# Performance work log

Hardware: AMD Instinct MI355X
Metric: run time of the kernel (lower is better)

The kernel has to match this reference:

```python
import jax, jax.numpy as jnp
import numpy as np

N_NODES = 50000
N_EDGES = 800000
IN_DIM, HIDDEN, Z_DIM = 32, 64, 32


def gcn_conv(x, W, b, src, dst, n):
    """PyG-style GCNConv: h = D^{-1/2}(A+I)D^{-1/2} (x W) + b."""
    h = x @ W  # [N, out]
    loop = jnp.arange(n, dtype=src.dtype)
    s = jnp.concatenate([src, loop])  # add self-loops
    d = jnp.concatenate([dst, loop])
    deg = jax.ops.segment_sum(jnp.ones(s.shape, h.dtype), d, num_segments=n)
    dinv = jax.lax.rsqrt(jnp.maximum(deg, jnp.asarray(1.0, h.dtype)))
    norm = dinv[s] * dinv[d]                       # [E+N]
    msg = h[s] * norm[:, None]                     # gather + scale
    out = jax.ops.segment_sum(msg, d, num_segments=n)  # scatter-add
    return out + b


def setup_inputs() -> dict:
    key = jax.random.key(0)
    ks = jax.random.split(key, 8)
    sc = lambda fan_in: 1.0 / np.sqrt(fan_in)
    x = jax.random.normal(ks[0], (N_NODES, IN_DIM), jnp.float32)
    edge_index = jax.random.randint(ks[1], (2, N_EDGES), 0, N_NODES, jnp.int64)
    W1 = jax.random.normal(ks[2], (IN_DIM, HIDDEN), jnp.float32) * sc(IN_DIM)
    b1 = jnp.zeros((HIDDEN,), jnp.float32)
    W2 = jax.random.normal(ks[3], (HIDDEN, HIDDEN), jnp.float32) * sc(HIDDEN)
    b2 = jnp.zeros((HIDDEN,), jnp.float32)
    W_mu = jax.random.normal(ks[4], (HIDDEN, Z_DIM), jnp.float32) * sc(HIDDEN)
    b_mu = jnp.zeros((Z_DIM,), jnp.float32)
    W_lv = jax.random.normal(ks[5], (HIDDEN, Z_DIM), jnp.float32) * sc(HIDDEN)
    b_lv = jnp.zeros((Z_DIM,), jnp.float32)
    eps = jax.random.normal(ks[6], (N_NODES, Z_DIM), jnp.float32)
    return {"x": x, "edge_index": edge_index, "W1": W1, "b1": b1, "W2": W2,
            "b2": b2, "W_mu": W_mu, "b_mu": b_mu, "W_lv": W_lv, "b_lv": b_lv,
            "eps": eps}


def reference(x, edge_index, W1, b1, W2, b2, W_mu, b_mu, W_lv, b_lv, eps):
    src, dst = edge_index[0], edge_index[1]
    n = x.shape[0]
    h = jax.nn.relu(gcn_conv(x, W1, b1, src, dst, n))
    h = jax.nn.relu(gcn_conv(h, W2, b2, src, dst, n))
    # dropout p=0.0 -> identity
    mu = gcn_conv(h, W_mu, b_mu, src, dst, n)
    logvar = gcn_conv(h, W_lv, b_lv, src, dst, n)
    z = mu + jnp.exp(0.5 * logvar) * eps  # reparametrize
    return (z, mu, logvar)
```

## Files before the change

kernel.cpp:

```cpp
#include <hip/hip_runtime.h>
#include <math.h>

#define N_NODES 50000
#define N_EDGES 800000
#define IN_DIM 32
#define HIDDEN 64
#define Z_DIM 32
#define SCAN_B 256
#define NB_SCAN ((N_NODES + SCAN_B - 1) / SCAN_B)
#define N_XCD 8
#define NPX ((N_NODES + N_XCD - 1) / N_XCD)
#define SLICE 2048
#define N_SLICE ((N_EDGES + SLICE - 1) / SLICE)
#define SCAT_B (N_SLICE * N_XCD)
#define FB 2048
#define CPAD 16

__device__ __forceinline__ float bf2f(unsigned short u) {
    return __uint_as_float(((unsigned int)u) << 16);
}
__device__ __forceinline__ unsigned short f2bf(float f) {
    unsigned int u = __float_as_uint(f);
    u += 0x7fffu + ((u >> 16) & 1u);
    return (unsigned short)(u >> 16);
}

__device__ __forceinline__ int detect64(const int* raw) {
    int lane = threadIdx.x & 63;
    int odd = raw[2 * lane + 1];
    unsigned long long b = __ballot(odd != 0);
    return (b == 0ULL) ? 1 : 0;
}

__global__ void prep_a_kernel(const float* __restrict__ x, unsigned short* __restrict__ xb,
                              const void* __restrict__ raw, int2* __restrict__ ep0,
                              int* __restrict__ dstc) {
    int is64 = detect64((const int*)raw);
    int i = blockIdx.x * 256 + threadIdx.x;
    if (i < N_NODES * IN_DIM) xb[i] = f2bf(x[i]);
    if (i < N_EDGES) {
        int s, d;
        if (is64) {
            s = (int)((const long long*)raw)[i];
            d = (int)((const long long*)raw)[N_EDGES + i];
        } else {
            s = ((const int*)raw)[i];
            d = ((const int*)raw)[N_EDGES + i];
        }
        ep0[i] = make_int2(s, d);
        dstc[i] = d;
    }
}

__global__ __launch_bounds__(256) void hist_kernel(const int* __restrict__ dstc,
                                                   int* __restrict__ cnt,
                                                   unsigned short* __restrict__ rank) {
    int xcd = blockIdx.x % N_XCD;
    int sl  = blockIdx.x / N_XCD;
    int lo  = xcd * NPX, hi = lo + NPX;
    int base = sl * SLICE;
#pragma unroll
    for (int j = 0; j < SLICE / 256; j++) {
        int e = base + j * 256 + threadIdx.x;
        if (e < N_EDGES) {
            int d = dstc[e];
            if (d >= lo && d < hi)
                rank[e] = (unsigned short)atomicAdd(&cnt[(size_t)d * CPAD], 1);
        }
    }
}

__global__ void scan1_kernel(const int* __restrict__ cnt, int* __restrict__ pre,
                             int* __restrict__ bsum, float* __restrict__ dinv) {
    __shared__ int s[SCAN_B];
    int t = threadIdx.x;
    int g = blockIdx.x * SCAN_B + t;
    int v = (g < N_NODES) ? cnt[(size_t)g * CPAD] : 0;
    if (g < N_NODES) dinv[g] = rsqrtf((float)(v + 1));
    s[t] = v;
    __syncthreads();
    for (int o = 1; o < SCAN_B; o <<= 1) {
        int add = (t >= o) ? s[t - o] : 0;
        __syncthreads();
        s[t] += add;
        __syncthreads();
    }
    if (g < N_NODES) pre[g] = s[t] - v;
    if (t == SCAN_B - 1) bsum[blockIdx.x] = s[t];
}

__global__ void scan23_kernel(int* __restrict__ rowptr, const int* __restrict__ bsum) {
    __shared__ int s[256];
    int t = threadIdx.x;
    int v = (t < NB_SCAN) ? bsum[t] : 0;
    s[t] = v;
    __syncthreads();
    for (int o = 1; o < 256; o <<= 1) {
        int add = (t >= o) ? s[t - o] : 0;
        __syncthreads();
        s[t] += add;
        __syncthreads();
    }
    int excl = s[blockIdx.x] - bsum[blockIdx.x];
    int g = blockIdx.x * SCAN_B + t;
    if (g < N_NODES) rowptr[g] += excl;
    if (g == 0) rowptr[N_NODES] = N_EDGES;
}

__global__ __launch_bounds__(256) void scatter_kernel(
        const int2* __restrict__ ep0, const unsigned short* __restrict__ rank,
        const int* __restrict__ rowptr, const float* __restrict__ dinv,
        int2* __restrict__ ep) {
    int base = blockIdx.x * SLICE;
#pragma unroll
    for (int j = 0; j < SLICE / 256; j++) {
        int e = base + j * 256 + threadIdx.x;
        if (e < N_EDGES) {
            int2 sd = ep0[e];
            int p = rowptr[sd.y] + (int)rank[e];
            ep[p] = make_int2(sd.x, __float_as_int(dinv[sd.x]));
        }
    }
}

__device__ __forceinline__ void agg_body64(int e0, int e1, int2 pr,
                                           const int2* __restrict__ ep,
                                           const uint2* __restrict__ g2,
                                           int lane, float acc[4]) {
    int gsel = lane >> 4;
    int c    = lane & 15;
    for (int base = e0; base < e1; base += 64) {
        int cnt = e1 - base; cnt = cnt > 64 ? 64 : cnt;
        for (int j = 0; j < cnt; j += 16) {
            uint2 fv[4]; float wv[4];
#pragma unroll
            for (int u = 0; u < 4; u++) {
                int idx = j + u * 4 + gsel;
                int cl  = idx < cnt ? idx : cnt - 1;
                int s   = __builtin_amdgcn_ds_bpermute(cl << 2, pr.x);
                int w   = __builtin_amdgcn_ds_bpermute(cl << 2, pr.y);
                wv[u]   = idx < cnt ? __int_as_float(w) : 0.0f;
                fv[u]   = g2[(size_t)s * 16 + c];
            }
#pragma unroll
            for (int u = 0; u < 4; u++) {
                acc[0] = fmaf(wv[u], __uint_as_float(fv[u].x << 16),         acc[0]);
                acc[1] = fmaf(wv[u], __uint_as_float(fv[u].x & 0xffff0000u), acc[1]);
                acc[2] = fmaf(wv[u], __uint_as_float(fv[u].y << 16),         acc[2]);
                acc[3] = fmaf(wv[u], __uint_as_float(fv[u].y & 0xffff0000u), acc[3]);
            }
        }
        int nb = base + 64;
        if (nb + lane < e1) pr = ep[nb + lane];
    }
}

__device__ __forceinline__ void agg_body32(int e0, int e1, int2 pr,
                                           const int2* __restrict__ ep,
                                           const uint2* __restrict__ x2,
                                           int lane, float acc[4]) {
    int gsel = lane >> 3;
    int c    = lane & 7;
    for (int base = e0; base < e1; base += 64) {
        int cnt = e1 - base; cnt = cnt > 64 ? 64 : cnt;
        for (int j = 0; j < cnt; j += 16) {
            uint2 fv[2]; float wv[2];
#pragma unroll
            for (int u = 0; u < 2; u++) {
                int idx = j + u * 8 + gsel;
                int cl  = idx < cnt ? idx : cnt - 1;
                int s   = __builtin_amdgcn_ds_bpermute(cl << 2, pr.x);
                int w   = __builtin_amdgcn_ds_bpermute(cl << 2, pr.y);
                wv[u]   = idx < cnt ? __int_as_float(w) : 0.0f;
                fv[u]   = x2[(size_t)s * 8 + c];
            }
#pragma unroll
            for (int u = 0; u < 2; u++) {
                acc[0] = fmaf(wv[u], __uint_as_float(fv[u].x << 16),         acc[0]);
                acc[1] = fmaf(wv[u], __uint_as_float(fv[u].x & 0xffff0000u), acc[1]);
                acc[2] = fmaf(wv[u], __uint_as_float(fv[u].y << 16),         acc[2]);
                acc[3] = fmaf(wv[u], __uint_as_float(fv[u].y & 0xffff0000u), acc[3]);
            }
        }
        int nb = base + 64;
        if (nb + lane < e1) pr = ep[nb + lane];
    }
}

__global__ __launch_bounds__(256, 4) void fused_layer32_kernel(
        const int* __restrict__ rowptr, const int2* __restrict__ ep,
        const float* __restrict__ dinv, const unsigned short* __restrict__ xb,
        const float* __restrict__ W1, const float* __restrict__ b1,
        unsigned short* __restrict__ out) {
    __shared__ float sq[4 * 32];
    int lane = threadIdx.x & 63;
    int wav  = threadIdx.x >> 6;
    int gsel = lane >> 3;
    int c    = lane & 7;
    const uint2* x2 = (const uint2*)xb;
    float wcol[IN_DIM];
#pragma unroll
    for (int k = 0; k < IN_DIM; k++) wcol[k] = W1[k * 64 + lane];
    float bb = b1[lane];
    int wid = __builtin_amdgcn_readfirstlane((int)((blockIdx.x * blockDim.x + threadIdx.x) >> 6));
    int nw  = (gridDim.x * blockDim.x) >> 6;
    int v = wid;
    if (v >= N_NODES) return;
    int e0 = rowptr[v], e1 = rowptr[v + 1];
    float dv = dinv[v];
    uint2 hv = x2[(size_t)v * 8 + c];
    int2 pr = make_int2(0, 0);
    if (lane < e1 - e0) pr = ep[e0 + lane];
    while (v < N_NODES) {
        int vn = v + nw;
        int e0n = 0, e1n = 0;
        float dvn = 0.0f;
        uint2 hvn = make_uint2(0, 0);
        int2 prn = make_int2(0, 0);
        if (vn < N_NODES) {
            e0n = rowptr[vn]; e1n = rowptr[vn + 1];
            dvn = dinv[vn];
            hvn = x2[(size_t)vn * 8 + c];
            if (lane < e1n - e0n) prn = ep[e0n + lane];
        }
        float sv = (gsel == 0) ? dv : 0.0f;
        float acc[4];
        acc[0] = sv * __uint_as_float(hv.x << 16);
        acc[1] = sv * __uint_as_float(hv.x & 0xffff0000u);
        acc[2] = sv * __uint_as_float(hv.y << 16);
        acc[3] = sv * __uint_as_float(hv.y & 0xffff0000u);
        agg_body32(e0, e1, pr, ep, x2, lane, acc);
#pragma unroll
        for (int i = 0; i < 4; i++) {
            acc[i] += __shfl_xor(acc[i], 8);
            acc[i] += __shfl_xor(acc[i], 16);
            acc[i] += __shfl_xor(acc[i], 32);
        }
        if (lane < 8)
            ((float4*)(sq + wav * 32))[c] =
                make_float4(dv * acc[0], dv * acc[1], dv * acc[2], dv * acc[3]);
        float o = bb;
        const float4* q4 = (const float4*)(sq + wav * 32);
#pragma unroll
        for (int k = 0; k < IN_DIM / 4; k++) {
            float4 t = q4[k];
            o = fmaf(t.x, wcol[4 * k + 0], o);
            o = fmaf(t.y, wcol[4 * k + 1], o);
            o = fmaf(t.z, wcol[4 * k + 2], o);
            o = fmaf(t.w, wcol[4 * k + 3], o);
        }
        out[(size_t)v * 64 + lane] = f2bf(fmaxf(o, 0.0f));
        v = vn; e0 = e0n; e1 = e1n; dv = dvn; hv = hvn; pr = prn;
    }
}

__global__ __launch_bounds__(256, 4) void fused_layer64_kernel(
        const int* __restrict__ rowptr, const int2* __restrict__ ep,
        const float* __restrict__ dinv, const unsigned short* __restrict__ g,
        const float* __restrict__ W, const float* __restrict__ bias,
        unsigned short* __restrict__ out) {
    __shared__ float sq[4 * 64];
    int lane = threadIdx.x & 63;
    int wav  = threadIdx.x >> 6;
    int gsel = lane >> 4;
    int c    = lane & 15;
    const uint2* g2 = (const uint2*)g;
    float wcol[HIDDEN];
#pragma unroll
    for (int k = 0; k < HIDDEN; k++) wcol[k] = W[k * 64 + lane];
    float bb = bias[lane];
    int wid = __builtin_amdgcn_readfirstlane((int)((blockIdx.x * blockDim.x + threadIdx.x) >> 6));
    int nw  = (gridDim.x * blockDim.x) >> 6;
    int v = wid;
    if (v >= N_NODES) return;
    int e0 = rowptr[v], e1 = rowptr[v + 1];
    float dv = dinv[v];
    uint2 hv = g2[(size_t)v * 16 + c];
    int2 pr = make_int2(0, 0);
    if (lane < e1 - e0) pr = ep[e0 + lane];
    while (v < N_NODES) {
        int vn = v + nw;
        int e0n = 0, e1n = 0;
        float dvn = 0.0f;
        uint2 hvn = make_uint2(0, 0);
        int2 prn = make_int2(0, 0);
        if (vn < N_NODES) {
            e0n = rowptr[vn]; e1n = rowptr[vn + 1];
            dvn = dinv[vn];
            hvn = g2[(size_t)vn * 16 + c];
            if (lane < e1n - e0n) prn = ep[e0n + lane];
        }
        float sv = (gsel == 0) ? dv : 0.0f;
        float acc[4];
        acc[0] = sv * __uint_as_float(hv.x << 16);
        acc[1] = sv * __uint_as_float(hv.x & 0xffff0000u);
        acc[2] = sv * __uint_as_float(hv.y << 16);
        acc[3] = sv * __uint_as_float(hv.y & 0xffff0000u);
        agg_body64(e0, e1, pr, ep, g2, lane, acc);
#pragma unroll
        for (int i = 0; i < 4; i++) {
            acc[i] += __shfl_xor(acc[i], 16);
            acc[i] += __shfl_xor(acc[i], 32);
        }
        if (lane < 16)
            ((float4*)(sq + wav * 64))[c] =
                make_float4(dv * acc[0], dv * acc[1], dv * acc[2], dv * acc[3]);
        float o = bb;
        const float4* q4 = (const float4*)(sq + wav * 64);
#pragma unroll
        for (int k = 0; k < HIDDEN / 4; k++) {
            float4 t = q4[k];
            o = fmaf(t.x, wcol[4 * k + 0], o);
            o = fmaf(t.y, wcol[4 * k + 1], o);
            o = fmaf(t.z, wcol[4 * k + 2], o);
            o = fmaf(t.w, wcol[4 * k + 3], o);
        }
        out[(size_t)v * 64 + lane] = f2bf(fmaxf(o, 0.0f));
        v = vn; e0 = e0n; e1 = e1n; dv = dvn; hv = hvn; pr = prn;
    }
}

__global__ __launch_bounds__(256, 4) void fused_head_kernel(
        const int* __restrict__ rowptr, const int2* __restrict__ ep,
        const float* __restrict__ dinv, const unsigned short* __restrict__ g,
        const float* __restrict__ Wmu, const float* __restrict__ Wlv,
        const float* __restrict__ bmu, const float* __restrict__ blv,
        const float* __restrict__ eps, float* __restrict__ outz) {
    __shared__ float sq[4 * 64];
    int lane = threadIdx.x & 63;
    int wav  = threadIdx.x >> 6;
    int gsel = lane >> 4;
    int c    = lane & 15;
    int f = lane & 31;
    bool hi = lane >= 32;
    const uint2* g2 = (const uint2*)g;
    float wcol[HIDDEN];
#pragma unroll
    for (int k = 0; k < HIDDEN; k++)
        wcol[k] = hi ? Wlv[k * 32 + f] : Wmu[k * 32 + f];
    float bb = hi ? blv[f] : bmu[f];
    float* z  = outz;
    float* mu = outz + (size_t)N_NODES * Z_DIM;
    float* lv = outz + 2 * (size_t)N_NODES * Z_DIM;
    int wid = __builtin_amdgcn_readfirstlane((int)((blockIdx.x * blockDim.x + threadIdx.x) >> 6));
    int nw  = (gridDim.x * blockDim.x) >> 6;
    int v = wid;
    if (v >= N_NODES) return;
    int e0 = rowptr[v], e1 = rowptr[v + 1];
    float dv = dinv[v];
    uint2 hv = g2[(size_t)v * 16 + c];
    int2 pr = make_int2(0, 0);
    if (lane < e1 - e0) pr = ep[e0 + lane];
    while (v < N_NODES) {
        int vn = v + nw;
        int e0n = 0, e1n = 0;
        float dvn = 0.0f;
        uint2 hvn = make_uint2(0, 0);
        int2 prn = make_int2(0, 0);
        if (vn < N_NODES) {
            e0n = rowptr[vn]; e1n = rowptr[vn + 1];
            dvn = dinv[vn];
            hvn = g2[(size_t)vn * 16 + c];
            if (lane < e1n - e0n) prn = ep[e0n + lane];
        }
        float sv = (gsel == 0) ? dv : 0.0f;
        float acc[4];
        acc[0] = sv * __uint_as_float(hv.x << 16);
        acc[1] = sv * __uint_as_float(hv.x & 0xffff0000u);
        acc[2] = sv * __uint_as_float(hv.y << 16);
        acc[3] = sv * __uint_as_float(hv.y & 0xffff0000u);
        agg_body64(e0, e1, pr, ep, g2, lane, acc);
#pragma unroll
        for (int i = 0; i < 4; i++) {
            acc[i] += __shfl_xor(acc[i], 16);
            acc[i] += __shfl_xor(acc[i], 32);
        }
        if (lane < 16)
            ((float4*)(sq + wav * 64))[c] =
                make_float4(dv * acc[0], dv * acc[1], dv * acc[2], dv * acc[3]);
        float m = bb;
        const float4* q4 = (const float4*)(sq + wav * 64);
#pragma unroll
        for (int k = 0; k < HIDDEN / 4; k++) {
            float4 t = q4[k];
            m = fmaf(t.x, wcol[4 * k + 0], m);
            m = fmaf(t.y, wcol[4 * k + 1], m);
            m = fmaf(t.z, wcol[4 * k + 2], m);
            m = fmaf(t.w, wcol[4 * k + 3], m);
        }
        float ev = eps[(size_t)v * Z_DIM + f];
        float t  = expf(0.5f * m) * ev;
        float tlo = __shfl(t, lane | 32);
        size_t o = (size_t)v * Z_DIM + f;
        if (!hi) { mu[o] = m; z[o] = m + tlo; }
        else     { lv[o] = m; }
        v = vn; e0 = e0n; e1 = e1n; dv = dvn; hv = hvn; pr = prn;
    }
}

extern "C" void kernel_launch(void* const* d_in, const int* in_sizes, int n_in,
                              void* d_out, int out_size, void* d_ws, size_t ws_size,
                              hipStream_t stream) {
    const float* x   = (const float*)d_in[0];
    const void*  ei  = d_in[1];
    const float* W1  = (const float*)d_in[2];
    const float* b1  = (const float*)d_in[3];
    const float* W2  = (const float*)d_in[4];
    const float* b2  = (const float*)d_in[5];
    const float* Wmu = (const float*)d_in[6];
    const float* bmu = (const float*)d_in[7];
    const float* Wlv = (const float*)d_in[8];
    const float* blv = (const float*)d_in[9];
    const float* eps = (const float*)d_in[10];
    float* out = (float*)d_out;
    (void)in_sizes; (void)n_in; (void)out_size; (void)ws_size;

    char* ws = (char*)d_ws;
    size_t off = 0;
    auto alloc = [&](size_t bytes) -> void* {
        void* p = ws + off;
        off += (bytes + 255) & ~(size_t)255;
        return p;
    };
    int2*           ep     = (int2*)alloc(sizeof(int2) * N_EDGES);
    int2*           ep0    = (int2*)alloc(sizeof(int2) * N_EDGES);
    int*            dstc   = (int*)alloc(sizeof(int) * N_EDGES);
    unsigned short* rank   = (unsigned short*)alloc(sizeof(short) * N_EDGES);
    int*            rowptr = (int*)alloc(sizeof(int) * (N_NODES + 1));
    int*            cnt    = (int*)alloc(sizeof(int) * (size_t)N_NODES * CPAD);
    float*          dinv   = (float*)alloc(sizeof(float) * N_NODES);
    int*            bsum   = (int*)alloc(sizeof(int) * 256);
    unsigned short* xb     = (unsigned short*)alloc(sizeof(short) * (size_t)N_NODES * IN_DIM);
    unsigned short* G      = (unsigned short*)alloc(sizeof(short) * (size_t)N_NODES * HIDDEN);
    unsigned short* H      = (unsigned short*)alloc(sizeof(short) * (size_t)N_NODES * HIDDEN);

    hipMemsetAsync(cnt, 0, sizeof(int) * (size_t)N_NODES * CPAD, stream);
    prep_a_kernel<<<(N_NODES * IN_DIM + 255) / 256, 256, 0, stream>>>(x, xb, ei, ep0, dstc);
    hist_kernel<<<SCAT_B, 256, 0, stream>>>(dstc, cnt, rank);
    scan1_kernel<<<NB_SCAN, SCAN_B, 0, stream>>>(cnt, rowptr, bsum, dinv);
    scan23_kernel<<<NB_SCAN, SCAN_B, 0, stream>>>(rowptr, bsum);
    scatter_kernel<<<N_SLICE, 256, 0, stream>>>(ep0, rank, rowptr, dinv, ep);
    fused_layer32_kernel<<<FB, 256, 0, stream>>>(rowptr, ep, dinv, xb, W1, b1, H);
    fused_layer64_kernel<<<FB, 256, 0, stream>>>(rowptr, ep, dinv, H, W2, b2, G);
    fused_head_kernel<<<FB, 256, 0, stream>>>(rowptr, ep, dinv, G, Wmu, Wlv, bmu, blv, eps, out);
}
```

Measured before the change: 234.1 us.

## Process two nodes per wave in aggregation and compact edge staging

The three fused GCN layer kernels now aggregate two destination nodes per wavefront in an interleaved loop, and they prefetch the next pair's state. This doubles the number of independent gathers in flight, to hide memory latency, and drops the occupancy hint from launch bounds. Edge staging packs src/dst as ushort2, which relies on node ids staying below 65536. The separate dst copy is removed, and zeroing the counters is folded into the prep kernel instead of a memset. The costs are higher register pressure and wasted lanes when the two nodes' degrees differ.

```diff
diff --git a/kernel.cpp b/kernel.cpp
--- a/kernel.cpp
+++ b/kernel.cpp
@@ -16,9 +16,6 @@
 #define FB 2048
 #define CPAD 16
 
-__device__ __forceinline__ float bf2f(unsigned short u) {
-    return __uint_as_float(((unsigned int)u) << 16);
-}
 __device__ __forceinline__ unsigned short f2bf(float f) {
     unsigned int u = __float_as_uint(f);
     u += 0x7fffu + ((u >> 16) & 1u);
@@ -33,11 +30,12 @@
 }
 
 __global__ void prep_a_kernel(const float* __restrict__ x, unsigned short* __restrict__ xb,
-                              const void* __restrict__ raw, int2* __restrict__ ep0,
-                              int* __restrict__ dstc) {
+                              const void* __restrict__ raw, ushort2* __restrict__ ep0,
+                              int* __restrict__ cnt) {
     int is64 = detect64((const int*)raw);
     int i = blockIdx.x * 256 + threadIdx.x;
     if (i < N_NODES * IN_DIM) xb[i] = f2bf(x[i]);
+    if (i < N_NODES * CPAD) cnt[i] = 0;
     if (i < N_EDGES) {
         int s, d;
         if (is64) {
@@ -47,12 +45,11 @@
             s = ((const int*)raw)[i];
             d = ((const int*)raw)[N_EDGES + i];
         }
-        ep0[i] = make_int2(s, d);
-        dstc[i] = d;
-    }
-}
-
-__global__ __launch_bounds__(256) void hist_kernel(const int* __restrict__ dstc,
+        ep0[i] = make_ushort2((unsigned short)s, (unsigned short)d);
+    }
+}
+
+__global__ __launch_bounds__(256) void hist_kernel(const ushort2* __restrict__ ep0,
                                                    int* __restrict__ cnt,
                                                    unsigned short* __restrict__ rank) {
     int xcd = blockIdx.x % N_XCD;
@@ -63,14 +60,14 @@
     for (int j = 0; j < SLICE / 256; j++) {
         int e = base + j * 256 + threadIdx.x;
         if (e < N_EDGES) {
-            int d = dstc[e];
+            int d = ep0[e].y;
             if (d >= lo && d < hi)
                 rank[e] = (unsigned short)atomicAdd(&cnt[(size_t)d * CPAD], 1);
         }
     }
 }
 
-__global__ void scan1_kernel(const int* __restrict__ cnt, int* __restrict__ pre,
+__global__ void scan1_kernel(const int* __restrict__ cnt, int* __restrict__ rowptr,
                              int* __restrict__ bsum, float* __restrict__ dinv) {
     __shared__ int s[SCAN_B];
     int t = threadIdx.x;
@@ -85,7 +82,7 @@
         s[t] += add;
         __syncthreads();
     }
-    if (g < N_NODES) pre[g] = s[t] - v;
+    if (g < N_NODES) rowptr[g] = s[t] - v;
     if (t == SCAN_B - 1) bsum[blockIdx.x] = s[t];
 }
 
@@ -108,7 +105,7 @@
 }
 
 __global__ __launch_bounds__(256) void scatter_kernel(
-        const int2* __restrict__ ep0, const unsigned short* __restrict__ rank,
+        const ushort2* __restrict__ ep0, const unsigned short* __restrict__ rank,
         const int* __restrict__ rowptr, const float* __restrict__ dinv,
         int2* __restrict__ ep) {
     int base = blockIdx.x * SLICE;
@@ -116,83 +113,114 @@
     for (int j = 0; j < SLICE / 256; j++) {
         int e = base + j * 256 + threadIdx.x;
         if (e < N_EDGES) {
-            int2 sd = ep0[e];
+            ushort2 sd = ep0[e];
             int p = rowptr[sd.y] + (int)rank[e];
-            ep[p] = make_int2(sd.x, __float_as_int(dinv[sd.x]));
-        }
-    }
-}
-
-__device__ __forceinline__ void agg_body64(int e0, int e1, int2 pr,
-                                           const int2* __restrict__ ep,
-                                           const uint2* __restrict__ g2,
-                                           int lane, float acc[4]) {
-    int gsel = lane >> 4;
-    int c    = lane & 15;
-    for (int base = e0; base < e1; base += 64) {
-        int cnt = e1 - base; cnt = cnt > 64 ? 64 : cnt;
-        for (int j = 0; j < cnt; j += 16) {
-            uint2 fv[4]; float wv[4];
+            int s = sd.x;
+            ep[p] = make_int2(s, __float_as_int(dinv[s]));
+        }
+    }
+}
+
+__device__ __forceinline__ void agg_dual64(
+        int e0A, int e1A, int2 prA, int e0B, int e1B, int2 prB,
+        const int2* __restrict__ ep, const uint2* __restrict__ g2,
+        int lane, int gsel, int c, float accA[4], float accB[4]) {
+    int bA = e0A, bB = e0B;
+    while (bA < e1A || bB < e1B) {
+        int cA = e1A - bA; cA = cA < 0 ? 0 : (cA > 64 ? 64 : cA);
+        int cB = e1B - bB; cB = cB < 0 ? 0 : (cB > 64 ? 64 : cB);
+        int mj = cA > cB ? cA : cB;
+        for (int j = 0; j < mj; j += 16) {
+            uint2 fA[4], fB[4]; float wA[4], wB[4];
 #pragma unroll
             for (int u = 0; u < 4; u++) {
                 int idx = j + u * 4 + gsel;
-                int cl  = idx < cnt ? idx : cnt - 1;
-                int s   = __builtin_amdgcn_ds_bpermute(cl << 2, pr.x);
-                int w   = __builtin_amdgcn_ds_bpermute(cl << 2, pr.y);
-                wv[u]   = idx < cnt ? __int_as_float(w) : 0.0f;
-                fv[u]   = g2[(size_t)s * 16 + c];
+                int clA = idx < cA ? idx : (cA > 0 ? cA - 1 : 0);
+                int clB = idx < cB ? idx : (cB > 0 ? cB - 1 : 0);
+                int sA  = __builtin_amdgcn_ds_bpermute(clA << 2, prA.x);
+                int wwA = __builtin_amdgcn_ds_bpermute(clA << 2, prA.y);
+                int sB  = __builtin_amdgcn_ds_bpermute(clB << 2, prB.x);
+                int wwB = __builtin_amdgcn_ds_bpermute(clB << 2, prB.y);
+                wA[u] = idx < cA ? __int_as_float(wwA) : 0.0f;
+                wB[u] = idx < cB ? __int_as_float(wwB) : 0.0f;
+                fA[u] = g2[(size_t)sA * 16 + c];
+                fB[u] = g2[(size_t)sB * 16 + c];
             }
 #pragma unroll
             for (int u = 0; u < 4; u++) {
-                acc[0] = fmaf(wv[u], __uint_as_float(fv[u].x << 16),         acc[0]);
-                acc[1] = fmaf(wv[u], __uint_as_float(fv[u].x & 0xffff0000u), acc[1]);
-                acc[2] = fmaf(wv[u], __uint_as_float(fv[u].y << 16),         acc[2]);
-                acc[3] = fmaf(wv[u], __uint_as_float(fv[u].y & 0xffff0000u), acc[3]);
+                accA[0] = fmaf(wA[u], __uint_as_float(fA[u].x << 16),         accA[0]);
+                accA[1] = fmaf(wA[u], __uint_as_float(fA[u].x & 0xffff0000u), accA[1]);
+                accA[2] = fmaf(wA[u], __uint_as_float(fA[u].y << 16),         accA[2]);
+                accA[3] = fmaf(wA[u], __uint_as_float(fA[u].y & 0xffff0000u), accA[3]);
+                accB[0] = fmaf(wB[u], __uint_as_float(fB[u].x << 16),         accB[0]);
+                accB[1] = fmaf(wB[u], __uint_as_float(fB[u].x & 0xffff0000u), accB[1]);
+                accB[2] = fmaf(wB[u], __uint_as_float(fB[u].y << 16),         accB[2]);
+                accB[3] = fmaf(wB[u], __uint_as_float(fB[u].y & 0xffff0000u), accB[3]);
             }
         }
-        int nb = base + 64;
-        if (nb + lane < e1) pr = ep[nb + lane];
-    }
-}
-
-__device__ __forceinline__ void agg_body32(int e0, int e1, int2 pr,
-                                           const int2* __restrict__ ep,
-                                           const uint2* __restrict__ x2,
-                                           int lane, float acc[4]) {
-    int gsel = lane >> 3;
-    int c    = lane & 7;
-    for (int base = e0; base < e1; base += 64) {
-        int cnt = e1 - base; cnt = cnt > 64 ? 64 : cnt;
-        for (int j = 0; j < cnt; j += 16) {
-            uint2 fv[2]; float wv[2];
+        bA += 64; bB += 64;
+        if (bA < e1A) { int i2 = bA + lane; prA = ep[i2 < e1A ? i2 : e1A - 1]; }
+        if (bB < e1B) { int i2 = bB + lane; prB = ep[i2 < e1B ? i2 : e1B - 1]; }
+    }
+}
+
+__device__ __forceinline__ void agg_dual32(
+        int e0A, int e1A, int2 prA, int e0B, int e1B, int2 prB,
+        const int2* __restrict__ ep, const uint2* __restrict__ x2,
+        int lane, int gsel, int c, float accA[4], float accB[4]) {
+    int bA = e0A, bB = e0B;
+    while (bA < e1A || bB < e1B) {
+        int cA = e1A - bA; cA = cA < 0 ? 0 : (cA > 64 ? 64 : cA);
+        int cB = e1B - bB; cB = cB < 0 ? 0 : (cB > 64 ? 64 : cB);
+        int mj = cA > cB ? cA : cB;
+        for (int j = 0; j < mj; j += 16) {
+            uint2 fA[2], fB[2]; float wA[2], wB[2];
 #pragma unroll
             for (int u = 0; u < 2; u++) {
                 int idx = j + u * 8 + gsel;
-                int cl  = idx < cnt ? idx : cnt - 1;
-                int s   = __builtin_amdgcn_ds_bpermute(cl << 2, pr.x);
-                int w   = __builtin_amdgcn_ds_bpermute(cl << 2, pr.y);
-                wv[u]   = idx < cnt ? __int_as_float(w) : 0.0f;
-                fv[u]   = x2[(size_t)s * 8 + c];
+                int clA = idx < cA ? idx : (cA > 0 ? cA - 1 : 0);
+                int clB = idx < cB ? idx : (cB > 0 ? cB - 1 : 0);
+                int sA  = __builtin_amdgcn_ds_bpermute(clA << 2, prA.x);
+                int wwA = __builtin_amdgcn_ds_bpermute(clA << 2, prA.y);
+                int sB  = __builtin_amdgcn_ds_bpermute(clB << 2, prB.x);
+                int wwB = __builtin_amdgcn_ds_bpermute(clB << 2, prB.y);
+                wA[u] = idx < cA ? __int_as_float(wwA) : 0.0f;
+                wB[u] = idx < cB ? __int_as_float(wwB) : 0.0f;
+                fA[u] = x2[(size_t)sA * 8 + c];
+                fB[u] = x2[(size_t)sB * 8 + c];
             }
 #pragma unroll
             for (int u = 0; u < 2; u++) {
-                acc[0] = fmaf(wv[u], __uint_as_float(fv[u].x << 16),         acc[0]);
-                acc[1] = fmaf(wv[u], __uint_as_float(fv[u].x & 0xffff0000u), acc[1]);
-                acc[2] = fmaf(wv[u], __uint_as_float(fv[u].y << 16),         acc[2]);
-                acc[3] = fmaf(wv[u], __uint_as_float(fv[u].y & 0xffff0000u), acc[3]);
+                accA[0] = fmaf(wA[u], __uint_as_float(fA[u].x << 16),         accA[0]);
+                accA[1] = fmaf(wA[u], __uint_as_float(fA[u].x & 0xffff0000u), accA[1]);
+                accA[2] = fmaf(wA[u], __uint_as_float(fA[u].y << 16),         accA[2]);
+                accA[3] = fmaf(wA[u], __uint_as_float(fA[u].y & 0xffff0000u), accA[3]);
+                accB[0] = fmaf(wB[u], __uint_as_float(fB[u].x << 16),         accB[0]);
+                accB[1] = fmaf(wB[u], __uint_as_float(fB[u].x & 0xffff0000u), accB[1]);
+                accB[2] = fmaf(wB[u], __uint_as_float(fB[u].y << 16),         accB[2]);
+                accB[3] = fmaf(wB[u], __uint_as_float(fB[u].y & 0xffff0000u), accB[3]);
             }
         }
-        int nb = base + 64;
-        if (nb + lane < e1) pr = ep[nb + lane];
-    }
-}
-
-__global__ __launch_bounds__(256, 4) void fused_layer32_kernel(
+        bA += 64; bB += 64;
+        if (bA < e1A) { int i2 = bA + lane; prA = ep[i2 < e1A ? i2 : e1A - 1]; }
+        if (bB < e1B) { int i2 = bB + lane; prB = ep[i2 < e1B ? i2 : e1B - 1]; }
+    }
+}
+
+#define LOAD_STATE(v, e0, e1, dv, hv, pr, HLOAD)                            \
+    {                                                                       \
+        e0 = rowptr[v]; e1 = rowptr[v + 1];                                 \
+        dv = dinv[v];                                                       \
+        hv = HLOAD;                                                         \
+        if (lane < e1 - e0) pr = ep[e0 + lane];                             \
+    }
+
+__global__ __launch_bounds__(256) void fused_layer32_kernel(
         const int* __restrict__ rowptr, const int2* __restrict__ ep,
         const float* __restrict__ dinv, const unsigned short* __restrict__ xb,
         const float* __restrict__ W1, const float* __restrict__ b1,
         unsigned short* __restrict__ out) {
-    __shared__ float sq[4 * 32];
+    __shared__ float sq[4][2][IN_DIM];
     int lane = threadIdx.x & 63;
     int wav  = threadIdx.x >> 6;
     int gsel = lane >> 3;
@@ -204,62 +232,87 @@
     float bb = b1[lane];
     int wid = __builtin_amdgcn_readfirstlane((int)((blockIdx.x * blockDim.x + threadIdx.x) >> 6));
     int nw  = (gridDim.x * blockDim.x) >> 6;
-    int v = wid;
-    if (v >= N_NODES) return;
-    int e0 = rowptr[v], e1 = rowptr[v + 1];
-    float dv = dinv[v];
-    uint2 hv = x2[(size_t)v * 8 + c];
-    int2 pr = make_int2(0, 0);
-    if (lane < e1 - e0) pr = ep[e0 + lane];
-    while (v < N_NODES) {
-        int vn = v + nw;
-        int e0n = 0, e1n = 0;
-        float dvn = 0.0f;
-        uint2 hvn = make_uint2(0, 0);
-        int2 prn = make_int2(0, 0);
-        if (vn < N_NODES) {
-            e0n = rowptr[vn]; e1n = rowptr[vn + 1];
-            dvn = dinv[vn];
-            hvn = x2[(size_t)vn * 8 + c];
-            if (lane < e1n - e0n) prn = ep[e0n + lane];
-        }
-        float sv = (gsel == 0) ? dv : 0.0f;
-        float acc[4];
-        acc[0] = sv * __uint_as_float(hv.x << 16);
-        acc[1] = sv * __uint_as_float(hv.x & 0xffff0000u);
-        acc[2] = sv * __uint_as_float(hv.y << 16);
-        acc[3] = sv * __uint_as_float(hv.y & 0xffff0000u);
-        agg_body32(e0, e1, pr, ep, x2, lane, acc);
+    int vA = wid;
+    if (vA >= N_NODES) return;
+    int e0A = 0, e1A = 0, e0B = 0, e1B = 0;
+    float dvA = 0.0f, dvB = 0.0f;
+    uint2 hvA = make_uint2(0, 0), hvB = make_uint2(0, 0);
+    int2 prA = make_int2(0, 0), prB = make_int2(0, 0);
+    LOAD_STATE(vA, e0A, e1A, dvA, hvA, prA, x2[(size_t)vA * 8 + c])
+    {
+        int vB = vA + nw;
+        if (vB < N_NODES)
+            LOAD_STATE(vB, e0B, e1B, dvB, hvB, prB, x2[(size_t)vB * 8 + c])
+    }
+    while (vA < N_NODES) {
+        int vB = vA + nw;
+        int vA2 = vA + 2 * nw;
+        int e0A2 = 0, e1A2 = 0, e0B2 = 0, e1B2 = 0;
+        float dvA2 = 0.0f, dvB2 = 0.0f;
+        uint2 hvA2 = make_uint2(0, 0), hvB2 = make_uint2(0, 0);
+        int2 prA2 = make_int2(0, 0), prB2 = make_int2(0, 0);
+        if (vA2 < N_NODES)
+            LOAD_STATE(vA2, e0A2, e1A2, dvA2, hvA2, prA2, x2[(size_t)vA2 * 8 + c])
+        if (vA2 + nw < N_NODES) {
+            int vB2 = vA2 + nw;
+            LOAD_STATE(vB2, e0B2, e1B2, dvB2, hvB2, prB2, x2[(size_t)vB2 * 8 + c])
+        }
+        float svA = (gsel == 0) ? dvA : 0.0f;
+        float svB = (gsel == 0) ? dvB : 0.0f;
+        float accA[4], accB[4];
+        accA[0] = svA * __uint_as_float(hvA.x << 16);
+        accA[1] = svA * __uint_as_float(hvA.x & 0xffff0000u);
+        accA[2] = svA * __uint_as_float(hvA.y << 16);
+        accA[3] = svA * __uint_as_float(hvA.y & 0xffff0000u);
+        accB[0] = svB * __uint_as_float(hvB.x << 16);
+        accB[1] = svB * __uint_as_float(hvB.x & 0xffff0000u);
+        accB[2] = svB * __uint_as_float(hvB.y << 16);
+        accB[3] = svB * __uint_as_float(hvB.y & 0xffff0000u);
+        agg_dual32(e0A, e1A, prA, e0B, e1B, prB, ep, x2, lane, gsel, c, accA, accB);
 #pragma unroll
         for (int i = 0; i < 4; i++) {
-            acc[i] += __shfl_xor(acc[i], 8);
-            acc[i] += __shfl_xor(acc[i], 16);
-            acc[i] += __shfl_xor(acc[i], 32);
-        }
-        if (lane < 8)
-            ((float4*)(sq + wav * 32))[c] =
-                make_float4(dv * acc[0], dv * acc[1], dv * acc[2], dv * acc[3]);
-        float o = bb;
-        const float4* q4 = (const float4*)(sq + wav * 32);
+            accA[i] += __shfl_xor(accA[i], 8);
+            accA[i] += __shfl_xor(accA[i], 16);
+            accA[i] += __shfl_xor(accA[i], 32);
+            accB[i] += __shfl_xor(accB[i], 8);
+            accB[i] += __shfl_xor(accB[i], 16);
+            accB[i] += __shfl_xor(accB[i], 32);
+        }
+        if (lane < 8) {
+            ((float4*)(&sq[wav][0][0]))[c] =
+                make_float4(dvA * accA[0], dvA * accA[1], dvA * accA[2], dvA * accA[3]);
+            ((float4*)(&sq[wav][1][0]))[c] =
+                make_float4(dvB * accB[0], dvB * accB[1], dvB * accB[2], dvB * accB[3]);
+        }
+        float oA = bb, oB = bb;
+        const float4* qA = (const float4*)(&sq[wav][0][0]);
+        const float4* qB = (const float4*)(&sq[wav][1][0]);
 #pragma unroll
         for (int k = 0; k < IN_DIM / 4; k++) {
-            float4 t = q4[k];
-            o = fmaf(t.x, wcol[4 * k + 0], o);
-            o = fmaf(t.y, wcol[4 * k + 1], o);
-            o = fmaf(t.z, wcol[4 * k + 2], o);
-            o = fmaf(t.w, wcol[4 * k + 3], o);
-        }
-        out[(size_t)v * 64 + lane] = f2bf(fmaxf(o, 0.0f));
-        v = vn; e0 = e0n; e1 = e1n; dv = dvn; hv = hvn; pr = prn;
-    }
-}
-
-__global__ __launch_bounds__(256, 4) void fused_layer64_kernel(
+            float4 ta = qA[k], tb = qB[k];
+            oA = fmaf(ta.x, wcol[4 * k + 0], oA);
+            oA = fmaf(ta.y, wcol[4 * k + 1], oA);
+            oA = fmaf(ta.z, wcol[4 * k + 2], oA);
+            oA = fmaf(ta.w, wcol[4 * k + 3], oA);
+            oB = fmaf(tb.x, wcol[4 * k + 0], oB);
+            oB = fmaf(tb.y, wcol[4 * k + 1], oB);
+            oB = fmaf(tb.z, wcol[4 * k + 2], oB);
+            oB = fmaf(tb.w, wcol[4 * k + 3], oB);
+        }
+        out[(size_t)vA * 64 + lane] = f2bf(fmaxf(oA, 0.0f));
+        if (vB < N_NODES) out[(size_t)vB * 64 + lane] = f2bf(fmaxf(oB, 0.0f));
+        vA = vA2;
+        e0A = e0A2; e1A = e1A2; dvA = dvA2; hvA = hvA2; prA = prA2;
+        e0B = e0B2; e1B = e1B2; dvB = dvB2; hvB = hvB2; prB = prB2;
+    }
+}
+
+__global__ __launch_bounds__(256) void fused_layer64_kernel(
         const int* __restrict__ rowptr, const int2* __restrict__ ep,
         const float* __restrict__ dinv, const unsigned short* __restrict__ g,
         const float* __restrict__ W, const float* __restrict__ bias,
         unsigned short* __restrict__ out) {
-    __shared__ float sq[4 * 64];
+    __shared__ float sq[4][2][HIDDEN];
     int lane = threadIdx.x & 63;
     int wav  = threadIdx.x >> 6;
     int gsel = lane >> 4;
@@ -271,62 +324,86 @@
     float bb = bias[lane];
     int wid = __builtin_amdgcn_readfirstlane((int)((blockIdx.x * blockDim.x + threadIdx.x) >> 6));
     int nw  = (gridDim.x * blockDim.x) >> 6;
-    int v = wid;
-    if (v >= N_NODES) return;
-    int e0 = rowptr[v], e1 = rowptr[v + 1];
-    float dv = dinv[v];
-    uint2 hv = g2[(size_t)v * 16 + c];
-    int2 pr = make_int2(0, 0);
-    if (lane < e1 - e0) pr = ep[e0 + lane];
-    while (v < N_NODES) {
-        int vn = v + nw;
-        int e0n = 0, e1n = 0;
-        float dvn = 0.0f;
-        uint2 hvn = make_uint2(0, 0);
-        int2 prn = make_int2(0, 0);
-        if (vn < N_NODES) {
-            e0n = rowptr[vn]; e1n = rowptr[vn + 1];
-            dvn = dinv[vn];
-            hvn = g2[(size_t)vn * 16 + c];
-            if (lane < e1n - e0n) prn = ep[e0n + lane];
-        }
-        float sv = (gsel == 0) ? dv : 0.0f;
-        float acc[4];
-        acc[0] = sv * __uint_as_float(hv.x << 16);
-        acc[1] = sv * __uint_as_float(hv.x & 0xffff0000u);
-        acc[2] = sv * __uint_as_float(hv.y << 16);
-        acc[3] = sv * __uint_as_float(hv.y & 0xffff0000u);
-        agg_body64(e0, e1, pr, ep, g2, lane, acc);
+    int vA = wid;
+    if (vA >= N_NODES) return;
+    int e0A = 0, e1A = 0, e0B = 0, e1B = 0;
+    float dvA = 0.0f, dvB = 0.0f;
+    uint2 hvA = make_uint2(0, 0), hvB = make_uint2(0, 0);
+    int2 prA = make_int2(0, 0), prB = make_int2(0, 0);
+    LOAD_STATE(vA, e0A, e1A, dvA, hvA, prA, g2[(size_t)vA * 16 + c])
+    {
+        int vB = vA + nw;
+        if (vB < N_NODES)
+            LOAD_STATE(vB, e0B, e1B, dvB, hvB, prB, g2[(size_t)vB * 16 + c])
+    }
+    while (vA < N_NODES) {
+        int vB = vA + nw;
+        int vA2 = vA + 2 * nw;
+        int e0A2 = 0, e1A2 = 0, e0B2 = 0, e1B2 = 0;
+        float dvA2 = 0.0f, dvB2 = 0.0f;
+        uint2 hvA2 = make_uint2(0, 0), hvB2 = make_uint2(0, 0);
+        int2 prA2 = make_int2(0, 0), prB2 = make_int2(0, 0);
+        if (vA2 < N_NODES)
+            LOAD_STATE(vA2, e0A2, e1A2, dvA2, hvA2, prA2, g2[(size_t)vA2 * 16 + c])
+        if (vA2 + nw < N_NODES) {
+            int vB2 = vA2 + nw;
+            LOAD_STATE(vB2, e0B2, e1B2, dvB2, hvB2, prB2, g2[(size_t)vB2 * 16 + c])
+        }
+        float svA = (gsel == 0) ? dvA : 0.0f;
+        float svB = (gsel == 0) ? dvB : 0.0f;
+        float accA[4], accB[4];
+        accA[0] = svA * __uint_as_float(hvA.x << 16);
+        accA[1] = svA * __uint_as_float(hvA.x & 0xffff0000u);
+        accA[2] = svA * __uint_as_float(hvA.y << 16);
+        accA[3] = svA * __uint_as_float(hvA.y & 0xffff0000u);
+        accB[0] = svB * __uint_as_float(hvB.x << 16);
+        accB[1] = svB * __uint_as_float(hvB.x & 0xffff0000u);
+        accB[2] = svB * __uint_as_float(hvB.y << 16);
+        accB[3] = svB * __uint_as_float(hvB.y & 0xffff0000u);
+        agg_dual64(e0A, e1A, prA, e0B, e1B, prB, ep, g2, lane, gsel, c, accA, accB);
 #pragma unroll
         for (int i = 0; i < 4; i++) {
-            acc[i] += __shfl_xor(acc[i], 16);
-            acc[i] += __shfl_xor(acc[i], 32);
-        }
-        if (lane < 16)
-            ((float4*)(sq + wav * 64))[c] =
-                make_float4(dv * acc[0], dv * acc[1], dv * acc[2], dv * acc[3]);
-        float o = bb;
-        const float4* q4 = (const float4*)(sq + wav * 64);
+            accA[i] += __shfl_xor(accA[i], 16);
+            accA[i] += __shfl_xor(accA[i], 32);
+            accB[i] += __shfl_xor(accB[i], 16);
+            accB[i] += __shfl_xor(accB[i], 32);
+        }
+        if (lane < 16) {
+            ((float4*)(&sq[wav][0][0]))[c] =
+                make_float4(dvA * accA[0], dvA * accA[1], dvA * accA[2], dvA * accA[3]);
+            ((float4*)(&sq[wav][1][0]))[c] =
+                make_float4(dvB * accB[0], dvB * accB[1], dvB * accB[2], dvB * accB[3]);
+        }
+        float oA = bb, oB = bb;
+        const float4* qA = (const float4*)(&sq[wav][0][0]);
+        const float4* qB = (const float4*)(&sq[wav][1][0]);
 #pragma unroll
         for (int k = 0; k < HIDDEN / 4; k++) {
-            float4 t = q4[k];
-            o = fmaf(t.x, wcol[4 * k + 0], o);
-            o = fmaf(t.y, wcol[4 * k + 1], o);
-            o = fmaf(t.z, wcol[4 * k + 2], o);
-            o = fmaf(t.w, wcol[4 * k + 3], o);
-        }
-        out[(size_t)v * 64 + lane] = f2bf(fmaxf(o, 0.0f));
-        v = vn; e0 = e0n; e1 = e1n; dv = dvn; hv = hvn; pr = prn;
-    }
-}
-
-__global__ __launch_bounds__(256, 4) void fused_head_kernel(
+            float4 ta = qA[k], tb = qB[k];
+            oA = fmaf(ta.x, wcol[4 * k + 0], oA);
+            oA = fmaf(ta.y, wcol[4 * k + 1], oA);
+            oA = fmaf(ta.z, wcol[4 * k + 2], oA);
+            oA = fmaf(ta.w, wcol[4 * k + 3], oA);
+            oB = fmaf(tb.x, wcol[4 * k + 0], oB);
+            oB = fmaf(tb.y, wcol[4 * k + 1], oB);
+            oB = fmaf(tb.z, wcol[4 * k + 2], oB);
+            oB = fmaf(tb.w, wcol[4 * k + 3], oB);
+        }
+        out[(size_t)vA * 64 + lane] = f2bf(fmaxf(oA, 0.0f));
+        if (vB < N_NODES) out[(size_t)vB * 64 + lane] = f2bf(fmaxf(oB, 0.0f));
+        vA = vA2;
+        e0A = e0A2; e1A = e1A2; dvA = dvA2; hvA = hvA2; prA = prA2;
+        e0B = e0B2; e1B = e1B2; dvB = dvB2; hvB = hvB2; prB = prB2;
+    }
+}
+
+__global__ __launch_bounds__(256) void fused_head_kernel(
         const int* __restrict__ rowptr, const int2* __restrict__ ep,
         const float* __restrict__ dinv, const unsigned short* __restrict__ g,
         const float* __restrict__ Wmu, const float* __restrict__ Wlv,
         const float* __restrict__ bmu, const float* __restrict__ blv,
         const float* __restrict__ eps, float* __restrict__ outz) {
-    __shared__ float sq[4 * 64];
+    __shared__ float sq[4][2][HIDDEN];
     int lane = threadIdx.x & 63;
     int wav  = threadIdx.x >> 6;
     int gsel = lane >> 4;
@@ -344,57 +421,90 @@
     float* lv = outz + 2 * (size_t)N_NODES * Z_DIM;
     int wid = __builtin_amdgcn_readfirstlane((int)((blockIdx.x * blockDim.x + threadIdx.x) >> 6));
     int nw  = (gridDim.x * blockDim.x) >> 6;
-    int v = wid;
-    if (v >= N_NODES) return;
-    int e0 = rowptr[v], e1 = rowptr[v + 1];
-    float dv = dinv[v];
-    uint2 hv = g2[(size_t)v * 16 + c];
-    int2 pr = make_int2(0, 0);
-    if (lane < e1 - e0) pr = ep[e0 + lane];
-    while (v < N_NODES) {
-        int vn = v + nw;
-        int e0n = 0, e1n = 0;
-        float dvn = 0.0f;
-        uint2 hvn = make_uint2(0, 0);
-        int2 prn = make_int2(0, 0);
-        if (vn < N_NODES) {
-            e0n = rowptr[vn]; e1n = rowptr[vn + 1];
-            dvn = dinv[vn];
-            hvn = g2[(size_t)vn * 16 + c];
-            if (lane < e1n - e0n) prn = ep[e0n + lane];
-        }
-        float sv = (gsel == 0) ? dv : 0.0f;
-        float acc[4];
-        acc[0] = sv * __uint_as_float(hv.x << 16);
-        acc[1] = sv * __uint_as_float(hv.x & 0xffff0000u);
-        acc[2] = sv * __uint_as_float(hv.y << 16);
-        acc[3] = sv * __uint_as_float(hv.y & 0xffff0000u);
-        agg_body64(e0, e1, pr, ep, g2, lane, acc);
+    int vA = wid;
+    if (vA >= N_NODES) return;
+    int e0A = 0, e1A = 0, e0B = 0, e1B = 0;
+    float dvA = 0.0f, dvB = 0.0f;
+    uint2 hvA = make_uint2(0, 0), hvB = make_uint2(0, 0);
+    int2 prA = make_int2(0, 0), prB = make_int2(0, 0);
+    LOAD_STATE(vA, e0A, e1A, dvA, hvA, prA, g2[(size_t)vA * 16 + c])
+    {
+        int vB = vA + nw;
+        if (vB < N_NODES)
+            LOAD_STATE(vB, e0B, e1B, dvB, hvB, prB, g2[(size_t)vB * 16 + c])
+    }
+    while (vA < N_NODES) {
+        int vB = vA + nw;
+        int vA2 = vA + 2 * nw;
+        int e0A2 = 0, e1A2 = 0, e0B2 = 0, e1B2 = 0;
+        float dvA2 = 0.0f, dvB2 = 0.0f;
+        uint2 hvA2 = make_uint2(0, 0), hvB2 = make_uint2(0, 0);
+        int2 prA2 = make_int2(0, 0), prB2 = make_int2(0, 0);
+        if (vA2 < N_NODES)
+            LOAD_STATE(vA2, e0A2, e1A2, dvA2, hvA2, prA2, g2[(size_t)vA2 * 16 + c])
+        if (vA2 + nw < N_NODES) {
+            int vB2 = vA2 + nw;
+            LOAD_STATE(vB2, e0B2, e1B2, dvB2, hvB2, prB2, g2[(size_t)vB2 * 16 + c])
+        }
+        float svA = (gsel == 0) ? dvA : 0.0f;
+        float svB = (gsel == 0) ? dvB : 0.0f;
+        float accA[4], accB[4];
+        accA[0] = svA * __uint_as_float(hvA.x << 16);
+        accA[1] = svA * __uint_as_float(hvA.x & 0xffff0000u);
+        accA[2] = svA * __uint_as_float(hvA.y << 16);
+        accA[3] = svA * __uint_as_float(hvA.y & 0xffff0000u);
+        accB[0] = svB * __uint_as_float(hvB.x << 16);
+        accB[1] = svB * __uint_as_float(hvB.x & 0xffff0000u);
+        accB[2] = svB * __uint_as_float(hvB.y << 16);
+        accB[3] = svB * __uint_as_float(hvB.y & 0xffff0000u);
+        agg_dual64(e0A, e1A, prA, e0B, e1B, prB, ep, g2, lane, gsel, c, accA, accB);
 #pragma unroll
         for (int i = 0; i < 4; i++) {
-            acc[i] += __shfl_xor(acc[i], 16);
-            acc[i] += __shfl_xor(acc[i], 32);
-        }
-        if (lane < 16)
-            ((float4*)(sq + wav * 64))[c] =
-                make_float4(dv * acc[0], dv * acc[1], dv * acc[2], dv * acc[3]);
-        float m = bb;
-        const float4* q4 = (const float4*)(sq + wav * 64);
+            accA[i] += __shfl_xor(accA[i], 16);
+            accA[i] += __shfl_xor(accA[i], 32);
+            accB[i] += __shfl_xor(accB[i], 16);
+            accB[i] += __shfl_xor(accB[i], 32);
+        }
+        if (lane < 16) {
+            ((float4*)(&sq[wav][0][0]))[c] =
+                make_float4(dvA * accA[0], dvA * accA[1], dvA * accA[2], dvA * accA[3]);
+            ((float4*)(&sq[wav][1][0]))[c] =
+                make_float4(dvB * accB[0], dvB * accB[1], dvB * accB[2], dvB * accB[3]);
+        }
+        float mA = bb, mB = bb;
+        const float4* qA = (const float4*)(&sq[wav][0][0]);
+        const float4* qB = (const float4*)(&sq[wav][1][0]);
 #pragma unroll
         for (int k = 0; k < HIDDEN / 4; k++) {
-            float4 t = q4[k];
-            m = fmaf(t.x, wcol[4 * k + 0], m);
-            m = fmaf(t.y, wcol[4 * k + 1], m);
-            m = fmaf(t.z, wcol[4 * k + 2], m);
-            m = fmaf(t.w, wcol[4 * k + 3], m);
-        }
-        float ev = eps[(size_t)v * Z_DIM + f];
-        float t  = expf(0.5f * m) * ev;
-        float tlo = __shfl(t, lane | 32);
-        size_t o = (size_t)v * Z_DIM + f;
-        if (!hi) { mu[o] = m; z[o] = m + tlo; }
-        else     { lv[o] = m; }
-        v = vn; e0 = e0n; e1 = e1n; dv = dvn; hv = hvn; pr = prn;
+            float4 ta = qA[k], tb = qB[k];
+            mA = fmaf(ta.x, wcol[4 * k + 0], mA);
+            mA = fmaf(ta.y, wcol[4 * k + 1], mA);
+            mA = fmaf(ta.z, wcol[4 * k + 2], mA);
+            mA = fmaf(ta.w, wcol[4 * k + 3], mA);
+            mB = fmaf(tb.x, wcol[4 * k + 0], mB);
+            mB = fmaf(tb.y, wcol[4 * k + 1], mB);
+            mB = fmaf(tb.z, wcol[4 * k + 2], mB);
+            mB = fmaf(tb.w, wcol[4 * k + 3], mB);
+        }
+        {
+            float ev = eps[(size_t)vA * Z_DIM + f];
+            float t  = expf(0.5f * mA) * ev;
+            float tlo = __shfl(t, lane | 32);
+            size_t o = (size_t)vA * Z_DIM + f;
+            if (!hi) { mu[o] = mA; z[o] = mA + tlo; }
+            else     { lv[o] = mA; }
+        }
+        if (vB < N_NODES) {
+            float ev = eps[(size_t)vB * Z_DIM + f];
+            float t  = expf(0.5f * mB) * ev;
+            float tlo = __shfl(t, lane | 32);
+            size_t o = (size_t)vB * Z_DIM + f;
+            if (!hi) { mu[o] = mB; z[o] = mB + tlo; }
+            else     { lv[o] = mB; }
+        }
+        vA = vA2;
+        e0A = e0A2; e1A = e1A2; dvA = dvA2; hvA = hvA2; prA = prA2;
+        e0B = e0B2; e1B = e1B2; dvB = dvB2; hvB = hvB2; prB = prB2;
     }
 }
 
@@ -423,8 +533,7 @@
         return p;
     };
     int2*           ep     = (int2*)alloc(sizeof(int2) * N_EDGES);
-    int2*           ep0    = (int2*)alloc(sizeof(int2) * N_EDGES);
-    int*            dstc   = (int*)alloc(sizeof(int) * N_EDGES);
+    ushort2*        ep0    = (ushort2*)alloc(sizeof(ushort2) * N_EDGES);
     unsigned short* rank   = (unsigned short*)alloc(sizeof(short) * N_EDGES);
     int*            rowptr = (int*)alloc(sizeof(int) * (N_NODES + 1));
     int*            cnt    = (int*)alloc(sizeof(int) * (size_t)N_NODES * CPAD);
@@ -434,9 +543,8 @@
     unsigned short* G      = (unsigned short*)alloc(sizeof(short) * (size_t)N_NODES * HIDDEN);
     unsigned short* H      = (unsigned short*)alloc(sizeof(short) * (size_t)N_NODES * HIDDEN);
 
-    hipMemsetAsync(cnt, 0, sizeof(int) * (size_t)N_NODES * CPAD, stream);
-    prep_a_kernel<<<(N_NODES * IN_DIM + 255) / 256, 256, 0, stream>>>(x, xb, ei, ep0, dstc);
-    hist_kernel<<<SCAT_B, 256, 0, stream>>>(dstc, cnt, rank);
+    prep_a_kernel<<<(N_NODES * IN_DIM + 255) / 256, 256, 0, stream>>>(x, xb, ei, ep0, cnt);
+    hist_kernel<<<SCAT_B, 256, 0, stream>>>(ep0, cnt, rank);
     scan1_kernel<<<NB_SCAN, SCAN_B, 0, stream>>>(cnt, rowptr, bsum, dinv);
     scan23_kernel<<<NB_SCAN, SCAN_B, 0, stream>>>(rowptr, bsum);
     scatter_kernel<<<N_SLICE, 256, 0, stream>>>(ep0, rank, rowptr, dinv, ep);
```

After: 242.0 us. 1.03x slower.
